# Optimization experiments

Hardware: AMD Instinct MI355X
Metric: run time of the kernel (lower is better)

Reference implementation:

```python
import jax, jax.numpy as jnp
import numpy as np

THRESHOLD = 1.0   # threshold_value
ALPHA = 2.0       # spikingjelly surrogate.ATan default alpha


@jax.custom_vjp
def spike(x):
    # Heaviside forward, ATan surrogate backward
    return (x >= 0.0).astype(x.dtype)

def _spike_fwd(x):
    return spike(x), x

def _spike_bwd(x, g):
    # d/dx [ (1/pi) * atan(pi/2 * alpha * x) + 1/2 ] = (alpha/2) / (1 + (pi/2*alpha*x)^2)
    return (g * (ALPHA / 2.0) / (1.0 + (jnp.pi / 2.0 * ALPHA * x) ** 2),)

spike.defvjp(_spike_fwd, _spike_bwd)


def _if_node(v, inp):
    # IFNode with v_reset=None (soft/residual reset): v += I; s = H(v - th); v -= s*th
    v = v + inp
    s = spike(v - THRESHOLD)
    v = v - s * THRESHOLD
    return v, s


def setup_inputs() -> dict:
    key = jax.random.key(0)
    ks = jax.random.split(key, 7)
    B, T = 1024, 128
    H1, H2, C = 512, 256, 18
    def lin(k, fan_out, fan_in):
        bound = 1.0 / np.sqrt(fan_in)
        kw, kb = jax.random.split(k)
        W = jax.random.uniform(kw, (fan_out, fan_in), jnp.float32, -bound, bound)
        b = jax.random.uniform(kb, (fan_out,), jnp.float32, -bound, bound)
        return W, b
    W1, b1 = lin(ks[0], H1, 1)
    W2, b2 = lin(ks[1], H2, H1)
    W3, b3 = lin(ks[2], C, H2)
    x = jax.random.normal(ks[3], (B, T), jnp.float32)
    return {"x": x, "W1": W1, "b1": b1, "W2": W2, "b2": b2,
            "W3": W3, "b3": b3, "repeat": 1}


def reference(x, W1, b1, W2, b2, W3, b3, repeat):
    B, T = x.shape
    H1, H2, C = W1.shape[0], W2.shape[0], W3.shape[0]

    def step(carry, xt):
        v1, v2, v3, acc = carry
        out = xt[:, None]                       # [B, 1]
        for _ in range(repeat):                  # original code only valid for repeat == 1
            v1, s1 = _if_node(v1, out @ W1.T + b1)   # [B, H1]
            v2, s2 = _if_node(v2, s1 @ W2.T + b2)    # [B, H2]
            v3, s3 = _if_node(v3, s2 @ W3.T + b3)    # [B, C]
            out = s3
        return (v1, v2, v3, acc + out), None

    z = lambda d: jnp.zeros((B, d), x.dtype)
    init = (z(H1), z(H2), z(C), z(C))
    (_, _, _, acc), _ = jax.lax.scan(step, init, x.T)   # scan over T timesteps
    return acc / T
```

## Files before the change

### kernel.cpp

```cpp
#include <hip/hip_runtime.h>
#include <cmath>

#define BB  1024
#define TT  128
#define HH1 512
#define HH2 256
#define CC  18

#define WS_DIG   0ull
#define WS_W3D   524288ull
#define WS_MASK  557056ull
#define WS_MASK2 8945664ull
#define WS_D3    13139968ull

typedef int  v4i  __attribute__((ext_vector_type(4)));
typedef int  v16i __attribute__((ext_vector_type(16)));
typedef unsigned long long ull;

__device__ __forceinline__ v4i expand_bits(unsigned bits) {
  v4i a;
  a.x = (int)((( bits        & 15u) * 0x204081u) & 0x01010101u);
  a.y = (int)((((bits >>  4) & 15u) * 0x204081u) & 0x01010101u);
  a.z = (int)((((bits >>  8) & 15u) * 0x204081u) & 0x01010101u);
  a.w = (int)((((bits >> 12) & 15u) * 0x204081u) & 0x01010101u);
  return a;
}

__global__ __launch_bounds__(256) void prep_weights(const float* __restrict__ W2,
    const float* __restrict__ W3, signed char* __restrict__ dig,
    signed char* __restrict__ w3dig)
{
  const int bid = blockIdx.x, tid = threadIdx.x;
  if (bid < 2048) {
    int i = bid * 256 + tid;
    int j = i & 15, n = (i >> 4) & 31, h = (i >> 9) & 1;
    int s = (i >> 10) & 15, d = (i >> 14) & 3, st = i >> 16;
    int h1 = s * 32 + h * 16 + j;
    int h2 = st * 32 + n;
    float w = W2[h2 * HH1 + h1];
    long long ll = llrint((double)w * 4294967296.0);
    int v = (int)ll;
    signed char d0 = (signed char)(v & 255); v = (v - d0) >> 8;
    signed char d1 = (signed char)(v & 255); v = (v - d1) >> 8;
    signed char d2 = (signed char)(v & 255); v = (v - d2) >> 8;
    signed char d3 = (signed char)v;
    dig[i] = (d == 0) ? d0 : (d == 1) ? d1 : (d == 2) ? d2 : d3;
  } else {
    int i = (bid - 2048) * 256 + tid;
    int j = i & 15, col = (i >> 4) & 31, h = (i >> 9) & 1;
    int c8 = (i >> 10) & 7, d = (i >> 13) & 3;
    int h2 = c8 * 32 + h * 16 + j;
    float w = (col < CC) ? W3[col * HH2 + h2] : 0.0f;
    long long ll = llrint((double)w * 4294967296.0);
    int v = (int)ll;
    signed char d0 = (signed char)(v & 255); v = (v - d0) >> 8;
    signed char d1 = (signed char)(v & 255); v = (v - d1) >> 8;
    signed char d2 = (signed char)(v & 255); v = (v - d2) >> 8;
    signed char d3 = (signed char)v;
    w3dig[i] = (d == 0) ? d0 : (d == 1) ? d1 : (d == 2) ? d2 : d3;
  }
}

__global__ __launch_bounds__(256) void phase_s1(const float* __restrict__ x,
    const float* __restrict__ W1, const float* __restrict__ b1,
    ull* __restrict__ masks)
{
  __shared__ float xrow[TT];
  int row = blockIdx.x, tid = threadIdx.x, wv = tid >> 6, lane = tid & 63;
  for (int i = tid; i < TT; i += 256) xrow[i] = x[row * TT + i];
  const float w1a = W1[tid], w1b = W1[tid + 256];
  const float b1a = b1[tid], b1b = b1[tid + 256];
  float v1a = 0.f, v1b = 0.f;
  __syncthreads();
  for (int t = 0; t < TT; ++t) {
    float xt = xrow[t];
    float iA = __fadd_rn(__fmul_rn(xt, w1a), b1a);
    v1a = __fadd_rn(v1a, iA);
    bool sA = (v1a >= 1.0f);  v1a = sA ? (v1a - 1.0f) : v1a;
    float iB = __fadd_rn(__fmul_rn(xt, w1b), b1b);
    v1b = __fadd_rn(v1b, iB);
    bool sB = (v1b >= 1.0f);  v1b = sB ? (v1b - 1.0f) : v1b;
    ull mA = __ballot(sA);
    ull mB = __ballot(sB);
    if (lane == 0) {
      ull* p = masks + (size_t)row * 1024 + (size_t)(t >> 5) * 256 + (t & 31);
      p[(size_t)wv * 32]       = mA;
      p[(size_t)(4 + wv) * 32] = mB;
    }
  }
}

__global__ __launch_bounds__(512, 2) void phase_gemmscan(
    const signed char* __restrict__ Bd, const ull* __restrict__ masks,
    const float* __restrict__ b2, unsigned* __restrict__ masks2)
{
  __shared__ __align__(16) signed char Bl[65536];

  const int bid = blockIdx.x;
  const int rowgrp = bid & 31, stripe = bid >> 5;
  const int tid = threadIdx.x, lane = tid & 63, wv = tid >> 6;
  const int half = lane >> 5, l31 = lane & 31;

  {
    const uint4* src = (const uint4*)(Bd + (size_t)stripe * 65536);
    uint4* dst = (uint4*)Bl;
#pragma unroll
    for (int i = 0; i < 8; ++i) dst[tid + 512 * i] = src[tid + 512 * i];
  }

  const signed char* bbase = Bl + half * 512 + l31 * 16;
  const float b2r = b2[stripe * 32 + l31];
  const unsigned hsh = half * 16;

  const int tp1 = (l31 & 3) + ((l31 >> 3) << 2) + ((l31 & 4) ? 16 : 0);
  const int tp2 = tp1 ^ 16;

  __syncthreads();

  if (wv & 4) {
    __builtin_amdgcn_s_sleep(15);
    __builtin_amdgcn_s_sleep(15);
  }

  for (int tau = 0; tau < 2; ++tau) {
    const int pr = wv + 8 * tau;
    const int r1 = rowgrp * 32 + 2 * pr;
    const ull* mb1 = masks + (size_t)r1 * 1024;
    const ull* mb2 = mb1 + 1024;
    unsigned* m2t = masks2 + (size_t)stripe * (TT * BB);
    float v2 = 0.f;

    ull wP[8], wQ[8], wPn[8], wQn[8];
#pragma unroll
    for (int k = 0; k < 8; ++k) {
      wP[k] = mb1[k * 32 + tp1];
      wQ[k] = mb2[k * 32 + tp2];
    }

#pragma unroll
    for (int c = 0; c < 4; ++c) {
      if (c < 3) {
#pragma unroll
        for (int k = 0; k < 8; ++k) {
          wPn[k] = mb1[(c + 1) * 256 + k * 32 + tp1];
          wQn[k] = mb2[(c + 1) * 256 + k * 32 + tp2];
        }
      }

      v16i aP[4], aQ[4];
#pragma unroll
      for (int d = 0; d < 4; ++d) {
        aP[d] = (v16i){0,0,0,0,0,0,0,0,0,0,0,0,0,0,0,0};
        aQ[d] = (v16i){0,0,0,0,0,0,0,0,0,0,0,0,0,0,0,0};
      }
      __builtin_amdgcn_s_setprio(1);
#pragma unroll
      for (int s = 0; s < 16; ++s) {
        v4i q0 = *(const v4i*)(bbase + (0 * 16 + s) * 1024);
        v4i q1 = *(const v4i*)(bbase + (1 * 16 + s) * 1024);
        v4i q2 = *(const v4i*)(bbase + (2 * 16 + s) * 1024);
        v4i q3 = *(const v4i*)(bbase + (3 * 16 + s) * 1024);
        unsigned shift = ((s & 1) << 5) + hsh;
        v4i eP = expand_bits((unsigned)(wP[s >> 1] >> shift) & 0xFFFFu);
        v4i eQ = expand_bits((unsigned)(wQ[s >> 1] >> shift) & 0xFFFFu);
        aP[0] = __builtin_amdgcn_mfma_i32_32x32x32_i8(eP, q0, aP[0], 0, 0, 0);
        aQ[0] = __builtin_amdgcn_mfma_i32_32x32x32_i8(eQ, q0, aQ[0], 0, 0, 0);
        aP[1] = __builtin_amdgcn_mfma_i32_32x32x32_i8(eP, q1, aP[1], 0, 0, 0);
        aQ[1] = __builtin_amdgcn_mfma_i32_32x32x32_i8(eQ, q1, aQ[1], 0, 0, 0);
        aP[2] = __builtin_amdgcn_mfma_i32_32x32x32_i8(eP, q2, aP[2], 0, 0, 0);
        aQ[2] = __builtin_amdgcn_mfma_i32_32x32x32_i8(eQ, q2, aQ[2], 0, 0, 0);
        aP[3] = __builtin_amdgcn_mfma_i32_32x32x32_i8(eP, q3, aP[3], 0, 0, 0);
        aQ[3] = __builtin_amdgcn_mfma_i32_32x32x32_i8(eQ, q3, aQ[3], 0, 0, 0);
      }
      __builtin_amdgcn_s_setprio(0);

      float dP[16], dQ[16];
#pragma unroll
      for (int r = 0; r < 16; ++r) {
        int sloP = aP[0][r] + (aP[1][r] << 8);
        int shiP = aP[2][r] + (aP[3][r] << 8);
        double ssP = fma((double)shiP, 65536.0, (double)sloP);
        dP[r] = (float)(ssP * 0x1p-32);
        int sloQ = aQ[0][r] + (aQ[1][r] << 8);
        int shiQ = aQ[2][r] + (aQ[3][r] << 8);
        double ssQ = fma((double)shiQ, 65536.0, (double)sloQ);
        dQ[r] = (float)(ssQ * 0x1p-32);
      }

      const int tb = c * 32;
#pragma unroll
      for (int r = 0; r < 16; ++r) {
        float val = half ? dQ[r] : dP[r];
        float i2 = __fadd_rn(val, b2r);
        v2 = __fadd_rn(v2, i2);
        bool s2 = (v2 >= 1.0f);  v2 = s2 ? (v2 - 1.0f) : v2;
        ull m = __ballot(s2);
        if (lane == 0)
          *(ull*)(m2t + (size_t)(tb + r) * BB + r1) = m;
      }
      v2 = __shfl_xor(v2, 32);
#pragma unroll
      for (int r = 0; r < 16; ++r) {
        float val = half ? dP[r] : dQ[r];
        float i2 = __fadd_rn(val, b2r);
        v2 = __fadd_rn(v2, i2);
        bool s2 = (v2 >= 1.0f);  v2 = s2 ? (v2 - 1.0f) : v2;
        ull m = __ballot(s2);
        if (lane == 0)
          *(ull*)(m2t + (size_t)(tb + 16 + r) * BB + r1) = (m >> 32) | (m << 32);
      }
      v2 = __shfl_xor(v2, 32);

      if (c < 3) {
#pragma unroll
        for (int k = 0; k < 8; ++k) { wP[k] = wPn[k]; wQ[k] = wQn[k]; }
      }
    }
  }
}

__global__ __launch_bounds__(256) void phase_l3(const signed char* __restrict__ W3d,
    const unsigned* __restrict__ masks2, float* __restrict__ D3)
{
  __shared__ __align__(16) signed char Bl[32768];
  const int bid = blockIdx.x;
  const int rowtile = bid & 31, tgrp = bid >> 5;
  const int tid = threadIdx.x, lane = tid & 63, wv = tid >> 6;
  const int half = lane >> 5;
  const int t = tgrp * 4 + wv;
  const int row = rowtile * 32 + (lane & 31);

  {
    const uint4* src = (const uint4*)W3d;
    uint4* dst = (uint4*)Bl;
#pragma unroll
    for (int i = 0; i < 8; ++i) dst[tid + 256 * i] = src[tid + 256 * i];
  }

  unsigned words[8];
  {
    const unsigned* mp = masks2 + (size_t)t * BB + row;
#pragma unroll
    for (int k = 0; k < 8; ++k) words[k] = mp[(size_t)k * (TT * BB)];
  }
  __syncthreads();

  const signed char* bbase = Bl + half * 512 + (lane & 31) * 16;
  v16i acc[4];
#pragma unroll
  for (int d = 0; d < 4; ++d) acc[d] = (v16i){0,0,0,0,0,0,0,0,0,0,0,0,0,0,0,0};

#pragma unroll
  for (int c8 = 0; c8 < 8; ++c8) {
    v4i a = expand_bits((words[c8] >> (half * 16)) & 0xFFFFu);
#pragma unroll
    for (int d = 0; d < 4; ++d) {
      v4i b = *(const v4i*)(bbase + ((d * 8 + c8) * 2) * 512);
      acc[d] = __builtin_amdgcn_mfma_i32_32x32x32_i8(a, b, acc[d], 0, 0, 0);
    }
  }

  const int col = lane & 31;
#pragma unroll
  for (int r = 0; r < 16; ++r) {
    int slo = acc[0][r] + (acc[1][r] << 8);
    int shi = acc[2][r] + (acc[3][r] << 8);
    double ss = fma((double)shi, 65536.0, (double)slo);
    float d3v = (float)(ss * 0x1p-32);
    int rowl = (r & 3) + 8 * (r >> 2) + 4 * half;
    int grow = rowtile * 32 + rowl;
    if (col < CC) D3[((size_t)t * BB + grow) * CC + col] = d3v;
  }
}

__global__ __launch_bounds__(128) void phase_v3(const float* __restrict__ D3,
    const float* __restrict__ b3, float* __restrict__ out)
{
  int g = blockIdx.x * 128 + threadIdx.x;
  int row = g / CC, c = g - row * CC; (void)row;
  const float b3r = b3[c];
  float v3 = 0.f, acc = 0.f;
  float cur[16], nxt[16];
#pragma unroll
  for (int p = 0; p < 16; ++p) cur[p] = D3[(size_t)p * (BB * CC) + g];
  for (int w = 0; w < 8; ++w) {
    if (w < 7) {
#pragma unroll
      for (int p = 0; p < 16; ++p)
        nxt[p] = D3[(size_t)((w + 1) * 16 + p) * (BB * CC) + g];
    }
#pragma unroll
    for (int p = 0; p < 16; ++p) {
      float i3 = __fadd_rn(cur[p], b3r);
      v3 = __fadd_rn(v3, i3);
      bool s3 = (v3 >= 1.0f);  v3 = s3 ? (v3 - 1.0f) : v3;
      acc = __fadd_rn(acc, s3 ? 1.0f : 0.0f);
    }
#pragma unroll
    for (int p = 0; p < 16; ++p) cur[p] = nxt[p];
  }
  out[g] = acc * (1.0f / TT);
}

extern "C" void kernel_launch(void* const* d_in, const int* in_sizes, int n_in,
                              void* d_out, int out_size, void* d_ws, size_t ws_size,
                              hipStream_t stream)
{
  (void)in_sizes; (void)n_in; (void)out_size; (void)ws_size;
  const float* x  = (const float*)d_in[0];
  const float* W1 = (const float*)d_in[1];
  const float* b1 = (const float*)d_in[2];
  const float* W2 = (const float*)d_in[3];
  const float* b2 = (const float*)d_in[4];
  const float* W3 = (const float*)d_in[5];
  const float* b3 = (const float*)d_in[6];
  float* out = (float*)d_out;
  char*  ws  = (char*)d_ws;

  signed char* dig    = (signed char*)(ws + WS_DIG);
  signed char* w3dig  = (signed char*)(ws + WS_W3D);
  ull*         masks  = (ull*)(ws + WS_MASK);
  unsigned*    masks2 = (unsigned*)(ws + WS_MASK2);
  float*       D3     = (float*)(ws + WS_D3);

  prep_weights<<<2176, 256, 0, stream>>>(W2, W3, dig, w3dig);
  phase_s1<<<1024, 256, 0, stream>>>(x, W1, b1, masks);
  phase_gemmscan<<<256, 512, 0, stream>>>(dig, masks, b2, masks2);
  phase_l3<<<1024, 256, 0, stream>>>(w3dig, masks2, D3);
  phase_v3<<<144, 128, 0, stream>>>(D3, b3, out);
}
```

Before: 182.1 us.

## Fuse layer-3 GEMM and membrane scan into one kernel with row-major spike masks

Changes the layer-2 spike mask layout to row-major per batch row (time x stripe words), and fuses the layer-3 int8 MFMA product with the layer-3 IF-neuron scan in one kernel, where each wave handles one batch row over all timesteps. This removes the D3 float intermediate's global write and read and one kernel launch. In exchange, the layer-3 kernel launches 256 blocks instead of 1024 and runs the time scan serially inside each wave, so latency and parallelism may suffer. The mask stores become 32-bit scattered writes from two lanes.

```diff
diff --git a/kernel.cpp b/kernel.cpp
--- a/kernel.cpp
+++ b/kernel.cpp
@@ -127,7 +127,6 @@
     const int r1 = rowgrp * 32 + 2 * pr;
     const ull* mb1 = masks + (size_t)r1 * 1024;
     const ull* mb2 = mb1 + 1024;
-    unsigned* m2t = masks2 + (size_t)stripe * (TT * BB);
     float v2 = 0.f;
 
     ull wP[8], wQ[8], wPn[8], wQn[8];
@@ -196,7 +195,10 @@
         bool s2 = (v2 >= 1.0f);  v2 = s2 ? (v2 - 1.0f) : v2;
         ull m = __ballot(s2);
         if (lane == 0)
-          *(ull*)(m2t + (size_t)(tb + r) * BB + r1) = m;
+          masks2[(size_t)r1 * 1024 + (size_t)(tb + r) * 8 + stripe] = (unsigned)m;
+        else if (lane == 32)
+          masks2[(size_t)(r1 + 1) * 1024 + (size_t)(tb + r) * 8 + stripe]
+              = (unsigned)(m >> 32);
       }
       v2 = __shfl_xor(v2, 32);
 #pragma unroll
@@ -207,7 +209,11 @@
         bool s2 = (v2 >= 1.0f);  v2 = s2 ? (v2 - 1.0f) : v2;
         ull m = __ballot(s2);
         if (lane == 0)
-          *(ull*)(m2t + (size_t)(tb + 16 + r) * BB + r1) = (m >> 32) | (m << 32);
+          masks2[(size_t)(r1 + 1) * 1024 + (size_t)(tb + 16 + r) * 8 + stripe]
+              = (unsigned)m;
+        else if (lane == 32)
+          masks2[(size_t)r1 * 1024 + (size_t)(tb + 16 + r) * 8 + stripe]
+              = (unsigned)(m >> 32);
       }
       v2 = __shfl_xor(v2, 32);
 
@@ -219,16 +225,14 @@
   }
 }
 
-__global__ __launch_bounds__(256) void phase_l3(const signed char* __restrict__ W3d,
-    const unsigned* __restrict__ masks2, float* __restrict__ D3)
+__global__ __launch_bounds__(256) void phase_l3v3(const signed char* __restrict__ W3d,
+    const unsigned* __restrict__ masks2, const float* __restrict__ b3,
+    float* __restrict__ out)
 {
   __shared__ __align__(16) signed char Bl[32768];
   const int bid = blockIdx.x;
-  const int rowtile = bid & 31, tgrp = bid >> 5;
   const int tid = threadIdx.x, lane = tid & 63, wv = tid >> 6;
-  const int half = lane >> 5;
-  const int t = tgrp * 4 + wv;
-  const int row = rowtile * 32 + (lane & 31);
+  const int half = lane >> 5, l31 = lane & 31;
 
   {
     const uint4* src = (const uint4*)W3d;
@@ -237,69 +241,73 @@
     for (int i = 0; i < 8; ++i) dst[tid + 256 * i] = src[tid + 256 * i];
   }
 
-  unsigned words[8];
-  {
-    const unsigned* mp = masks2 + (size_t)t * BB + row;
-#pragma unroll
-    for (int k = 0; k < 8; ++k) words[k] = mp[(size_t)k * (TT * BB)];
-  }
+  const int row = bid * 4 + wv;
+  const unsigned* mrow = masks2 + (size_t)row * (TT * 8);
+  const signed char* bbase = Bl + half * 512 + l31 * 16;
+  const float b3r = b3[l31 < CC ? l31 : 0];
+  const unsigned hsh = half * 16;
+  const int tp1 = (l31 & 3) + ((l31 >> 3) << 2) + ((l31 & 4) ? 16 : 0);
+
   __syncthreads();
 
-  const signed char* bbase = Bl + half * 512 + (lane & 31) * 16;
-  v16i acc[4];
-#pragma unroll
-  for (int d = 0; d < 4; ++d) acc[d] = (v16i){0,0,0,0,0,0,0,0,0,0,0,0,0,0,0,0};
-
-#pragma unroll
-  for (int c8 = 0; c8 < 8; ++c8) {
-    v4i a = expand_bits((words[c8] >> (half * 16)) & 0xFFFFu);
-#pragma unroll
-    for (int d = 0; d < 4; ++d) {
-      v4i b = *(const v4i*)(bbase + ((d * 8 + c8) * 2) * 512);
-      acc[d] = __builtin_amdgcn_mfma_i32_32x32x32_i8(a, b, acc[d], 0, 0, 0);
-    }
-  }
-
-  const int col = lane & 31;
-#pragma unroll
-  for (int r = 0; r < 16; ++r) {
-    int slo = acc[0][r] + (acc[1][r] << 8);
-    int shi = acc[2][r] + (acc[3][r] << 8);
-    double ss = fma((double)shi, 65536.0, (double)slo);
-    float d3v = (float)(ss * 0x1p-32);
-    int rowl = (r & 3) + 8 * (r >> 2) + 4 * half;
-    int grow = rowtile * 32 + rowl;
-    if (col < CC) D3[((size_t)t * BB + grow) * CC + col] = d3v;
-  }
-}
-
-__global__ __launch_bounds__(128) void phase_v3(const float* __restrict__ D3,
-    const float* __restrict__ b3, float* __restrict__ out)
-{
-  int g = blockIdx.x * 128 + threadIdx.x;
-  int row = g / CC, c = g - row * CC; (void)row;
-  const float b3r = b3[c];
-  float v3 = 0.f, acc = 0.f;
-  float cur[16], nxt[16];
-#pragma unroll
-  for (int p = 0; p < 16; ++p) cur[p] = D3[(size_t)p * (BB * CC) + g];
-  for (int w = 0; w < 8; ++w) {
-    if (w < 7) {
-#pragma unroll
-      for (int p = 0; p < 16; ++p)
-        nxt[p] = D3[(size_t)((w + 1) * 16 + p) * (BB * CC) + g];
-    }
-#pragma unroll
-    for (int p = 0; p < 16; ++p) {
-      float i3 = __fadd_rn(cur[p], b3r);
-      v3 = __fadd_rn(v3, i3);
-      bool s3 = (v3 >= 1.0f);  v3 = s3 ? (v3 - 1.0f) : v3;
-      acc = __fadd_rn(acc, s3 ? 1.0f : 0.0f);
-    }
-#pragma unroll
-    for (int p = 0; p < 16; ++p) cur[p] = nxt[p];
-  }
-  out[g] = acc * (1.0f / TT);
+  float v3 = 0.f, ac = 0.f;
+
+  for (int c = 0; c < 4; ++c) {
+    unsigned w8[8];
+    {
+      const unsigned* mp = mrow + (size_t)(c * 32 + tp1) * 8;
+      *(uint4*)&w8[0] = *(const uint4*)mp;
+      *(uint4*)&w8[4] = *(const uint4*)(mp + 4);
+    }
+
+    v16i acc[4];
+#pragma unroll
+    for (int d = 0; d < 4; ++d)
+      acc[d] = (v16i){0,0,0,0,0,0,0,0,0,0,0,0,0,0,0,0};
+
+#pragma unroll
+    for (int c8 = 0; c8 < 8; ++c8) {
+      v4i e = expand_bits((w8[c8] >> hsh) & 0xFFFFu);
+#pragma unroll
+      for (int d = 0; d < 4; ++d) {
+        v4i b = *(const v4i*)(bbase + (d * 8 + c8) * 1024);
+        acc[d] = __builtin_amdgcn_mfma_i32_32x32x32_i8(e, b, acc[d], 0, 0, 0);
+      }
+    }
+
+    float dv[16];
+#pragma unroll
+    for (int r = 0; r < 16; ++r) {
+      int slo = acc[0][r] + (acc[1][r] << 8);
+      int shi = acc[2][r] + (acc[3][r] << 8);
+      double ss = fma((double)shi, 65536.0, (double)slo);
+      dv[r] = (float)(ss * 0x1p-32);
+    }
+
+#pragma unroll
+    for (int r = 0; r < 16; ++r) {
+      float i3 = __fadd_rn(dv[r], b3r);
+      float u  = __fadd_rn(v3, i3);
+      bool s3  = (u >= 1.0f);
+      float uv = s3 ? (u - 1.0f) : u;
+      float av = __fadd_rn(ac, s3 ? 1.0f : 0.0f);
+      if (!half) { v3 = uv; ac = av; }
+    }
+    v3 = __shfl_xor(v3, 32); ac = __shfl_xor(ac, 32);
+#pragma unroll
+    for (int r = 0; r < 16; ++r) {
+      float i3 = __fadd_rn(dv[r], b3r);
+      float u  = __fadd_rn(v3, i3);
+      bool s3  = (u >= 1.0f);
+      float uv = s3 ? (u - 1.0f) : u;
+      float av = __fadd_rn(ac, s3 ? 1.0f : 0.0f);
+      if (half) { v3 = uv; ac = av; }
+    }
+    v3 = __shfl_xor(v3, 32); ac = __shfl_xor(ac, 32);
+  }
+
+  if (!half && l31 < CC)
+    out[row * CC + l31] = ac * (1.0f / TT);
 }
 
 extern "C" void kernel_launch(void* const* d_in, const int* in_sizes, int n_in,
@@ -321,11 +329,9 @@
   signed char* w3dig  = (signed char*)(ws + WS_W3D);
   ull*         masks  = (ull*)(ws + WS_MASK);
   unsigned*    masks2 = (unsigned*)(ws + WS_MASK2);
-  float*       D3     = (float*)(ws + WS_D3);
 
   prep_weights<<<2176, 256, 0, stream>>>(W2, W3, dig, w3dig);
   phase_s1<<<1024, 256, 0, stream>>>(x, W1, b1, masks);
   phase_gemmscan<<<256, 512, 0, stream>>>(dig, masks, b2, masks2);
-  phase_l3<<<1024, 256, 0, stream>>>(w3dig, masks2, D3);
-  phase_v3<<<144, 128, 0, stream>>>(D3, b3, out);
-}
+  phase_l3v3<<<256, 256, 0, stream>>>(w3dig, masks2, b3, out);
+}
```

Result: no change. 185.6 us (+2.0%).
